# Optimization experiments

Hardware: AMD Instinct MI355X
Metric: run time of the kernel (lower is better)

The kernel has to match this reference:

```python
import jax, jax.numpy as jnp
import numpy as np

B, T, D, H = 8192, 1024, 16, 16

def setup_inputs() -> dict:
    key = jax.random.key(0)
    k1, k2, k3, k4 = jax.random.split(key, 4)
    x = jax.random.normal(k1, (B, T, D), dtype=jnp.float32)
    # fused LSTM params: gate order (i, f, g, o)
    Wi = jax.random.normal(k2, (D, 4 * H), dtype=jnp.float32) * (1.0 / np.sqrt(D))
    Wh = jax.random.normal(k3, (H, 4 * H), dtype=jnp.float32) * (1.0 / np.sqrt(H))
    b = jnp.zeros((4 * H,), dtype=jnp.float32)
    Wd = jax.random.normal(k4, (H, 2), dtype=jnp.float32) * (1.0 / np.sqrt(H))
    bd = jnp.zeros((2,), dtype=jnp.float32)
    return {"x": x, "Wi": Wi, "Wh": Wh, "b": b, "Wd": Wd, "bd": bd}

def reference(x, Wi, Wh, b, Wd, bd):
    Bx = x.shape[0]
    Hh = Wh.shape[0]
    c0 = jnp.zeros((Bx, Hh), dtype=x.dtype)
    h0 = jnp.zeros((Bx, Hh), dtype=x.dtype)

    def step(carry, x_t):
        c, h = carry
        z = x_t @ Wi + h @ Wh + b  # [B, 4H]
        i, f, g, o = jnp.split(z, 4, axis=-1)
        c = jax.nn.sigmoid(f) * c + jax.nn.sigmoid(i) * jnp.tanh(g)
        h = jax.nn.sigmoid(o) * jnp.tanh(c)
        return (c, h), None

    (c_T, h_T), _ = jax.lax.scan(step, (c0, h0), jnp.swapaxes(x, 0, 1))
    # NOTE: the original flax model uses carry1[0], the CELL state c, for the head
    logits = c_T @ Wd + bd
    return jax.nn.softmax(logits, axis=-1)
```

## Files before the change

kernel.cpp:

```cpp
#include <hip/hip_runtime.h>
#include <math.h>


#define BB 8192
#define TT 1024
#define DD 16
#define HH 16

__device__ __forceinline__ float fast_sigmoid(float x) {
    return __builtin_amdgcn_rcpf(1.0f + __expf(-x));
}
__device__ __forceinline__ float fast_tanh(float x) {
    return 1.0f - 2.0f * __builtin_amdgcn_rcpf(1.0f + __expf(2.0f * x));
}

__global__ __launch_bounds__(256, 2) void carry_lstm_kernel(
    const float* __restrict__ x,
    const float* __restrict__ Wi,
    const float* __restrict__ Wh,
    const float* __restrict__ b,
    const float* __restrict__ Wd,
    const float* __restrict__ bd,
    float* __restrict__ out)
{
    const int tid = blockIdx.x * blockDim.x + threadIdx.x;
    const int e = tid >> 4;
    const int u = tid & 15;

    float wI[DD][4], wH[HH][4];
#pragma unroll
    for (int k = 0; k < DD; ++k) {
#pragma unroll
        for (int g = 0; g < 4; ++g) {
            wI[k][g] = Wi[k * 64 + g * 16 + u];
            wH[k][g] = Wh[k * 64 + g * 16 + u];
        }
    }
    float bz[4];
#pragma unroll
    for (int g = 0; g < 4; ++g) bz[g] = b[g * 16 + u];

    const float4* xv = (const float4*)(x + (size_t)e * (TT * DD));

    float c = 0.0f;
    float hb[HH];
#pragma unroll
    for (int k = 0; k < HH; ++k) hb[k] = 0.0f;

    float4 xa = xv[0], xb = xv[1], xc = xv[2], xd = xv[3];

    for (int t = 0; t < TT; ++t) {
        const int tn = (t + 1 < TT) ? (t + 1) : (TT - 1);
        const float4* nxt = xv + tn * 4;
        float4 na = nxt[0], nb = nxt[1], nc = nxt[2], nd = nxt[3];

        const float xin[DD] = {xa.x, xa.y, xa.z, xa.w,
                               xb.x, xb.y, xb.z, xb.w,
                               xc.x, xc.y, xc.z, xc.w,
                               xd.x, xd.y, xd.z, xd.w};

        float z0 = bz[0], z1 = bz[1], z2 = bz[2], z3 = bz[3];
#pragma unroll
        for (int k = 0; k < DD; ++k) {
            z0 = fmaf(xin[k], wI[k][0], z0);
            z1 = fmaf(xin[k], wI[k][1], z1);
            z2 = fmaf(xin[k], wI[k][2], z2);
            z3 = fmaf(xin[k], wI[k][3], z3);
        }
#pragma unroll
        for (int k = 0; k < HH; ++k) {
            z0 = fmaf(hb[k], wH[k][0], z0);
            z1 = fmaf(hb[k], wH[k][1], z1);
            z2 = fmaf(hb[k], wH[k][2], z2);
            z3 = fmaf(hb[k], wH[k][3], z3);
        }

        const float ig = fast_sigmoid(z0);
        const float fg = fast_sigmoid(z1);
        const float gg = fast_tanh(z2);
        const float og = fast_sigmoid(z3);
        c = fmaf(fg, c, ig * gg);
        const float h = og * fast_tanh(c);

#pragma unroll
        for (int k = 0; k < HH; ++k) hb[k] = __shfl(h, k, 16);

        xa = na; xb = nb; xc = nc; xd = nd;
    }

    float p0 = c * Wd[u * 2 + 0];
    float p1 = c * Wd[u * 2 + 1];
#pragma unroll
    for (int off = 8; off >= 1; off >>= 1) {
        p0 += __shfl_xor(p0, off, 16);
        p1 += __shfl_xor(p1, off, 16);
    }
    if (u == 0) {
        const float l0 = p0 + bd[0];
        const float l1 = p1 + bd[1];
        const float m = fmaxf(l0, l1);
        const float e0 = __expf(l0 - m);
        const float e1 = __expf(l1 - m);
        const float inv = __builtin_amdgcn_rcpf(e0 + e1);
        out[e * 2 + 0] = e0 * inv;
        out[e * 2 + 1] = e1 * inv;
    }
}

extern "C" void kernel_launch(void* const* d_in, const int* in_sizes, int n_in,
                              void* d_out, int out_size, void* d_ws, size_t ws_size,
                              hipStream_t stream) {
    const float* x  = (const float*)d_in[0];
    const float* Wi = (const float*)d_in[1];
    const float* Wh = (const float*)d_in[2];
    const float* b  = (const float*)d_in[3];
    const float* Wd = (const float*)d_in[4];
    const float* bd = (const float*)d_in[5];
    float* out = (float*)d_out;

    dim3 grid(BB * 16 / 256);
    dim3 block(256);
    hipLaunchKernelGGL(carry_lstm_kernel, grid, block, 0, stream,
                       x, Wi, Wh, b, Wd, bd, out);
}
```

Measured before the change: 1.215 ms.

## Rewrite LSTM recurrence with bf16 MFMA per 16-sequence wavefront

Replaces the per-thread scalar FMA gate computation with a single wavefront handling 16 sequences, using bf16 16x16x32 MFMA over concatenated [x_t, h_{t-1}] against packed Wi/Wh. The hidden state and input are exchanged through LDS in bf16, and the gate nonlinearities are algebraically fused into fewer exps and one reciprocal per cell update. The aim is to take the gate matmul off the VALU, which dominates the old loop's FMA count. It trades precision (bf16 weights, inputs and hidden state, clamped exponents) and relies on wavefront-lockstep LDS ordering with only compiler barriers.

```diff
diff --git a/kernel.cpp b/kernel.cpp
--- a/kernel.cpp
+++ b/kernel.cpp
@@ -1,5 +1,6 @@
 #include <hip/hip_runtime.h>
 #include <math.h>
+#include <stdint.h>
 
 
 #define BB 8192
@@ -7,14 +8,16 @@
 #define DD 16
 #define HH 16
 
-__device__ __forceinline__ float fast_sigmoid(float x) {
-    return __builtin_amdgcn_rcpf(1.0f + __expf(-x));
-}
-__device__ __forceinline__ float fast_tanh(float x) {
-    return 1.0f - 2.0f * __builtin_amdgcn_rcpf(1.0f + __expf(2.0f * x));
+typedef __attribute__((ext_vector_type(8))) short short8;
+typedef __attribute__((ext_vector_type(4))) float f32x4;
+
+__device__ __forceinline__ short f2bf(float f) {
+    uint32_t u = __builtin_bit_cast(uint32_t, f);
+    u += 0x7fffu + ((u >> 16) & 1u);
+    return (short)(u >> 16);
 }
 
-__global__ __launch_bounds__(256, 2) void carry_lstm_kernel(
+__global__ __launch_bounds__(64) void carry_lstm_mfma(
     const float* __restrict__ x,
     const float* __restrict__ Wi,
     const float* __restrict__ Wh,
@@ -23,87 +26,115 @@
     const float* __restrict__ bd,
     float* __restrict__ out)
 {
-    const int tid = blockIdx.x * blockDim.x + threadIdx.x;
-    const int e = tid >> 4;
-    const int u = tid & 15;
+    __shared__ __align__(16) char smem[1536];
+    const int lane = threadIdx.x;
+    const int n = lane & 15;
+    const int q = lane >> 4;
+    const int e0 = blockIdx.x * 16;
 
-    float wI[DD][4], wH[HH][4];
+    short8 Bg[4];
+    float bias[4];
 #pragma unroll
-    for (int k = 0; k < DD; ++k) {
+    for (int g = 0; g < 4; ++g) {
 #pragma unroll
-        for (int g = 0; g < 4; ++g) {
-            wI[k][g] = Wi[k * 64 + g * 16 + u];
-            wH[k][g] = Wh[k * 64 + g * 16 + u];
+        for (int j = 0; j < 8; ++j) {
+            const int row = q * 8 + j;
+            const float w = (row < 16) ? Wi[row * 64 + g * 16 + n]
+                                       : Wh[(row - 16) * 64 + g * 16 + n];
+            Bg[g][j] = f2bf(w);
+        }
+        bias[g] = b[g * 16 + n];
+    }
+
+    const float* xg = x + (size_t)(e0 + n) * (TT * DD) + q * 4;
+    char* xw = &smem[n * 48 + q * 8];
+    const short8* afp = (const short8*)&smem[(q >> 1) * 768 + n * 48 + (q & 1) * 16];
+
+    *(uint2*)&smem[768 + n * 48 + q * 8] = make_uint2(0u, 0u);
+    {
+        float4 x0 = *(const float4*)(xg);
+        uint32_t lo = (uint16_t)f2bf(x0.x) | ((uint32_t)(uint16_t)f2bf(x0.y) << 16);
+        uint32_t hi = (uint16_t)f2bf(x0.z) | ((uint32_t)(uint16_t)f2bf(x0.w) << 16);
+        *(uint2*)xw = make_uint2(lo, hi);
+    }
+    float4 xf = *(const float4*)(xg + DD);
+
+    float cr[4] = {0.f, 0.f, 0.f, 0.f};
+
+    for (int t = 0; t < TT; ++t) {
+        short8 af = *afp;
+        asm volatile("" ::: "memory");
+
+        f32x4 acc0 = {bias[0], bias[0], bias[0], bias[0]};
+        f32x4 acc1 = {bias[1], bias[1], bias[1], bias[1]};
+        f32x4 acc2 = {bias[2], bias[2], bias[2], bias[2]};
+        f32x4 acc3 = {bias[3], bias[3], bias[3], bias[3]};
+        acc0 = __builtin_amdgcn_mfma_f32_16x16x32_bf16(af, Bg[0], acc0, 0, 0, 0);
+        acc1 = __builtin_amdgcn_mfma_f32_16x16x32_bf16(af, Bg[1], acc1, 0, 0, 0);
+        acc2 = __builtin_amdgcn_mfma_f32_16x16x32_bf16(af, Bg[2], acc2, 0, 0, 0);
+        acc3 = __builtin_amdgcn_mfma_f32_16x16x32_bf16(af, Bg[3], acc3, 0, 0, 0);
+
+        const int t2 = (t + 2 < TT) ? (t + 2) : (TT - 1);
+        const float4 xf2 = *(const float4*)(xg + (size_t)t2 * DD);
+
+#pragma unroll
+        for (int r = 0; r < 4; ++r) {
+            float zi = acc0[r], zf = acc1[r], zg = acc2[r], zo = acc3[r];
+            zi = fmaxf(zi, -12.f); zf = fmaxf(zf, -12.f);
+            zg = fmaxf(zg, -12.f); zo = fmaxf(zo, -12.f);
+            const float ea = __expf(-zi);
+            const float ef = __expf(-zf);
+            const float G  = __expf(-2.f * zg);
+            const float eo = __expf(-zo);
+            float u = fmaf(cr[r], ea, cr[r]);
+            u = fmaf(u, G, u);
+            const float s  = 1.f - G;
+            const float s2 = fmaf(s, ef, s);
+            const float num = u + s2;
+            const float den = ((ea + 1.f) * (ef + 1.f));
+            const float den3 = fmaf(den, G, den);
+            const float cn = num * __builtin_amdgcn_rcpf(den3);
+            cr[r] = cn;
+            const float cc = fmaxf(cn, -12.f);
+            const float C2 = __expf(-2.f * cc);
+            const float hd = (1.f + C2) * (1.f + eo);
+            const float h  = (1.f - C2) * __builtin_amdgcn_rcpf(hd);
+            *(short*)&smem[768 + (q * 4 + r) * 48 + n * 2] = f2bf(h);
+        }
+
+        {
+            uint32_t lo = (uint16_t)f2bf(xf.x) | ((uint32_t)(uint16_t)f2bf(xf.y) << 16);
+            uint32_t hi = (uint16_t)f2bf(xf.z) | ((uint32_t)(uint16_t)f2bf(xf.w) << 16);
+            *(uint2*)xw = make_uint2(lo, hi);
+        }
+        xf = xf2;
+        asm volatile("" ::: "memory");
+    }
+
+    float p0[4], p1[4];
+    const float wd0 = Wd[n * 2 + 0], wd1 = Wd[n * 2 + 1];
+#pragma unroll
+    for (int r = 0; r < 4; ++r) { p0[r] = cr[r] * wd0; p1[r] = cr[r] * wd1; }
+#pragma unroll
+    for (int off = 1; off < 16; off <<= 1) {
+#pragma unroll
+        for (int r = 0; r < 4; ++r) {
+            p0[r] += __shfl_xor(p0[r], off, 16);
+            p1[r] += __shfl_xor(p1[r], off, 16);
         }
     }
-    float bz[4];
 #pragma unroll
-    for (int g = 0; g < 4; ++g) bz[g] = b[g * 16 + u];
-
-    const float4* xv = (const float4*)(x + (size_t)e * (TT * DD));
-
-    float c = 0.0f;
-    float hb[HH];
-#pragma unroll
-    for (int k = 0; k < HH; ++k) hb[k] = 0.0f;
-
-    float4 xa = xv[0], xb = xv[1], xc = xv[2], xd = xv[3];
-
-    for (int t = 0; t < TT; ++t) {
-        const int tn = (t + 1 < TT) ? (t + 1) : (TT - 1);
-        const float4* nxt = xv + tn * 4;
-        float4 na = nxt[0], nb = nxt[1], nc = nxt[2], nd = nxt[3];
-
-        const float xin[DD] = {xa.x, xa.y, xa.z, xa.w,
-                               xb.x, xb.y, xb.z, xb.w,
-                               xc.x, xc.y, xc.z, xc.w,
-                               xd.x, xd.y, xd.z, xd.w};
-
-        float z0 = bz[0], z1 = bz[1], z2 = bz[2], z3 = bz[3];
-#pragma unroll
-        for (int k = 0; k < DD; ++k) {
-            z0 = fmaf(xin[k], wI[k][0], z0);
-            z1 = fmaf(xin[k], wI[k][1], z1);
-            z2 = fmaf(xin[k], wI[k][2], z2);
-            z3 = fmaf(xin[k], wI[k][3], z3);
+    for (int r = 0; r < 4; ++r) {
+        if (n == r) {
+            const float l0 = p0[r] + bd[0];
+            const float l1 = p1[r] + bd[1];
+            const float m  = fmaxf(l0, l1);
+            const float E0 = __expf(l0 - m), E1 = __expf(l1 - m);
+            const float inv = __builtin_amdgcn_rcpf(E0 + E1);
+            const size_t e = (size_t)(e0 + q * 4 + r);
+            out[e * 2 + 0] = E0 * inv;
+            out[e * 2 + 1] = E1 * inv;
         }
-#pragma unroll
-        for (int k = 0; k < HH; ++k) {
-            z0 = fmaf(hb[k], wH[k][0], z0);
-            z1 = fmaf(hb[k], wH[k][1], z1);
-            z2 = fmaf(hb[k], wH[k][2], z2);
-            z3 = fmaf(hb[k], wH[k][3], z3);
-        }
-
-        const float ig = fast_sigmoid(z0);
-        const float fg = fast_sigmoid(z1);
-        const float gg = fast_tanh(z2);
-        const float og = fast_sigmoid(z3);
-        c = fmaf(fg, c, ig * gg);
-        const float h = og * fast_tanh(c);
-
-#pragma unroll
-        for (int k = 0; k < HH; ++k) hb[k] = __shfl(h, k, 16);
-
-        xa = na; xb = nb; xc = nc; xd = nd;
-    }
-
-    float p0 = c * Wd[u * 2 + 0];
-    float p1 = c * Wd[u * 2 + 1];
-#pragma unroll
-    for (int off = 8; off >= 1; off >>= 1) {
-        p0 += __shfl_xor(p0, off, 16);
-        p1 += __shfl_xor(p1, off, 16);
-    }
-    if (u == 0) {
-        const float l0 = p0 + bd[0];
-        const float l1 = p1 + bd[1];
-        const float m = fmaxf(l0, l1);
-        const float e0 = __expf(l0 - m);
-        const float e1 = __expf(l1 - m);
-        const float inv = __builtin_amdgcn_rcpf(e0 + e1);
-        out[e * 2 + 0] = e0 * inv;
-        out[e * 2 + 1] = e1 * inv;
     }
 }
 
@@ -118,8 +149,6 @@
     const float* bd = (const float*)d_in[5];
     float* out = (float*)d_out;
 
-    dim3 grid(BB * 16 / 256);
-    dim3 block(256);
-    hipLaunchKernelGGL(carry_lstm_kernel, grid, block, 0, stream,
+    hipLaunchKernelGGL(carry_lstm_mfma, dim3(BB / 16), dim3(64), 0, stream,
                        x, Wi, Wh, b, Wd, bd, out);
 }
```

New measurement: 1.181 ms. 1.03x faster.
